# Performance work log

Hardware: AMD Instinct MI355X
Metric: run time of the kernel (lower is better)

The kernel has to match this reference:

```python
import jax, jax.numpy as jnp
import numpy as np

EPS = 1e-5


def _selective_scan(u, delta, A, Bm, Cm, D, delta_bias):
    # u, delta: (B, KD, L); A: (KD, N); Bm, Cm: (B, K, N, L); D, delta_bias: (KD,)
    Bb, KD, L = u.shape
    K = Bm.shape[1]
    Din = KD // K
    N = A.shape[1]
    delta = jax.nn.softplus(delta + delta_bias[None, :, None])            # (B,KD,L)
    dA = jnp.exp(delta[..., None] * A[None, :, None, :])                  # (B,KD,L,N)
    Bl = jnp.broadcast_to(Bm[:, :, None], (Bb, K, Din, N, L)).reshape(Bb, KD, N, L)
    Bl = jnp.moveaxis(Bl, -1, 2)                                          # (B,KD,L,N)
    dBu = (delta * u)[..., None] * Bl                                     # (B,KD,L,N)

    def comb(c1, c2):
        a1, b1 = c1
        a2, b2 = c2
        return a2 * a1, a2 * b1 + b2

    _, h = jax.lax.associative_scan(comb, (dA, dBu), axis=2)              # h: (B,KD,L,N)
    Cl = jnp.broadcast_to(Cm[:, :, None], (Bb, K, Din, N, L)).reshape(Bb, KD, N, L)
    Cl = jnp.moveaxis(Cl, -1, 2)
    y = jnp.sum(h * Cl, axis=-1) + D[None, :, None] * u                   # (B,KD,L)
    return y


def setup_inputs() -> dict:
    key = jax.random.key(0)
    ks = jax.random.split(key, 12)
    B, H, W, Dd = 1, 16, 16, 16
    C = 48            # d_model
    Din = 48          # d_inner (expand=1)
    N = 16            # d_state
    R = 3             # dt_rank = ceil(48/16)
    K = 8             # scan directions
    x = jax.random.normal(ks[0], (B, H, W, Dd, C), jnp.float32)
    in_proj_w = jax.random.normal(ks[1], (2 * Din, C), jnp.float32) * (C ** -0.5)
    conv_w = jax.random.normal(ks[2], (Din, 1, 3, 3, 3), jnp.float32) * 0.1
    conv_b = jax.random.normal(ks[3], (Din,), jnp.float32) * 0.01
    x_proj_weight = jax.random.normal(ks[4], (K, R + 2 * N, Din), jnp.float32) * (Din ** -0.5)
    dt_projs_weight = jax.random.uniform(ks[5], (K, Din, R), jnp.float32, -(R ** -0.5), R ** -0.5)
    # faithful dt bias init: inverse softplus of dt ~ logU(1e-3, 1e-1)
    u = jax.random.uniform(ks[6], (K, Din), jnp.float32)
    dt = jnp.exp(u * (np.log(0.1) - np.log(0.001)) + np.log(0.001))
    dt = jnp.clip(dt, 1e-4, None)
    dt_projs_bias = dt + jnp.log(-jnp.expm1(-dt))
    A_logs = jnp.log(jnp.broadcast_to(jnp.arange(1, N + 1, dtype=jnp.float32), (K * Din, N))).copy()
    Ds = jnp.ones((K * Din,), jnp.float32)
    norm_w = jnp.ones((Din,), jnp.float32)
    norm_b = jnp.zeros((Din,), jnp.float32)
    out_proj_w = jax.random.normal(ks[7], (C, Din), jnp.float32) * (Din ** -0.5)
    return {"x": x, "in_proj_w": in_proj_w, "conv_w": conv_w, "conv_b": conv_b,
            "x_proj_weight": x_proj_weight, "dt_projs_weight": dt_projs_weight,
            "dt_projs_bias": dt_projs_bias, "A_logs": A_logs, "Ds": Ds,
            "norm_w": norm_w, "norm_b": norm_b, "out_proj_w": out_proj_w}


def reference(x, in_proj_w, conv_w, conv_b, x_proj_weight, dt_projs_weight,
              dt_projs_bias, A_logs, Ds, norm_w, norm_b, out_proj_w):
    Bb, H, W, Dd, C = x.shape
    Din = in_proj_w.shape[0] // 2
    K = x_proj_weight.shape[0]
    R = dt_projs_weight.shape[2]
    N = A_logs.shape[1]
    L = H * W * Dd
    # in_proj and gate split
    xz = jnp.einsum('bhwdc,ec->bhwde', x, in_proj_w)
    xm, z = jnp.split(xz, 2, axis=-1)
    # depthwise 3D conv + SiLU (channels-first)
    xc = jnp.transpose(xm, (0, 4, 1, 2, 3))                               # (B,Din,H,W,D)
    xc = jax.lax.conv_general_dilated(xc, conv_w, (1, 1, 1), 'SAME',
                                      dimension_numbers=('NCDHW', 'OIDHW', 'NCDHW'),
                                      feature_group_count=Din)
    xc = jax.nn.silu(xc + conv_b[None, :, None, None, None])
    # 8 scan orderings: 4 axis permutations + their reversals
    x0 = xc.reshape(Bb, Din, L)
    x1 = jnp.transpose(xc, (0, 1, 3, 2, 4)).reshape(Bb, Din, L)
    x2 = jnp.transpose(xc, (0, 1, 4, 3, 2)).reshape(Bb, Din, L)
    x3 = jnp.transpose(xc, (0, 1, 2, 4, 3)).reshape(Bb, Din, L)
    x4s = jnp.stack([x0, x1, x2, x3], axis=1)                             # (B,4,Din,L)
    xs = jnp.concatenate([x4s, jnp.flip(x4s, axis=-1)], axis=1)           # (B,8,Din,L)
    # per-direction projections
    x_dbl = jnp.einsum('bkdl,kcd->bkcl', xs, x_proj_weight)
    dts, Bs, Cs = jnp.split(x_dbl, [R, R + N], axis=2)                    # (B,K,R,L),(B,K,N,L),(B,K,N,L)
    dts = jnp.einsum('bkrl,kdr->bkdl', dts, dt_projs_weight)              # (B,K,Din,L)
    u = xs.reshape(Bb, K * Din, L)
    delta = dts.reshape(Bb, K * Din, L)
    A = -jnp.exp(A_logs)                                                  # (K*Din, N)
    y = _selective_scan(u, delta, A, Bs, Cs, Ds, dt_projs_bias.reshape(-1))
    y = y.reshape(Bb, K, Din, L)
    # undo reversals and permutations, sum all directions
    yk = y[:, :4] + jnp.flip(y[:, 4:], axis=-1)                           # (B,4,Din,L)
    y0 = yk[:, 0].reshape(Bb, Din, H, W, Dd)
    y1 = jnp.transpose(yk[:, 1].reshape(Bb, Din, W, H, Dd), (0, 1, 3, 2, 4))
    y2 = jnp.transpose(yk[:, 2].reshape(Bb, Din, Dd, W, H), (0, 1, 4, 3, 2))
    y3 = jnp.transpose(yk[:, 3].reshape(Bb, Din, H, Dd, W), (0, 1, 2, 4, 3))
    ysum = y0 + y1 + y2 + y3                                              # (B,Din,H,W,D)
    # LayerNorm over channels, gate, out_proj
    yl = jnp.transpose(ysum, (0, 2, 3, 4, 1))                             # (B,H,W,D,Din)
    mu = jnp.mean(yl, axis=-1, keepdims=True)
    var = jnp.mean((yl - mu) ** 2, axis=-1, keepdims=True)
    yn = (yl - mu) * jax.lax.rsqrt(var + EPS) * norm_w + norm_b
    out = yn * jax.nn.silu(z)
    return jnp.einsum('bhwde,ce->bhwdc', out, out_proj_w)
```

## Files before the change

### kernel.cpp

```cpp
#include <hip/hip_runtime.h>
#include <hip/hip_bf16.h>
#include <math.h>

#define HH 16
#define WW 16
#define DD 16
#define LL 4096
#define CC 48
#define DIN 48
#define NN 16
#define RR 3
#define KK 8
#define KD 384
#define NCH 64
#define CHL 64

__device__ __forceinline__ float dpp_add(float x, const int ctrl_tag) {
    int xi = __float_as_int(x);
    int yi;
    switch (ctrl_tag) {
        case 0: yi = __builtin_amdgcn_update_dpp(0, xi, 0xB1, 0xF, 0xF, true); break;
        case 1: yi = __builtin_amdgcn_update_dpp(0, xi, 0x4E, 0xF, 0xF, true); break;
        case 2: yi = __builtin_amdgcn_update_dpp(0, xi, 0x124, 0xF, 0xF, true); break;
        default: yi = __builtin_amdgcn_update_dpp(0, xi, 0x128, 0xF, 0xF, true); break;
    }
    return x + __int_as_float(yi);
}
__device__ __forceinline__ float row16_sum(float p) {
    p = dpp_add(p, 0);
    p = dpp_add(p, 1);
    p = dpp_add(p, 2);
    p = dpp_add(p, 3);
    return p;
}

__global__ __launch_bounds__(256) void k_inproj(const float* __restrict__ x,
                                                const float* __restrict__ W,
                                                float* __restrict__ xm,
                                                float* __restrict__ z) {
    int tid = blockIdx.x * 256 + threadIdx.x;
    if (tid >= LL * 96) return;
    int e = tid % 96, l = tid / 96;
    const float4* xr = (const float4*)(x + l * CC);
    const float4* wr = (const float4*)(W + e * CC);
    float acc = 0.f;
#pragma unroll
    for (int c4 = 0; c4 < CC / 4; ++c4) {
        float4 a = xr[c4], b = wr[c4];
        acc += a.x * b.x + a.y * b.y + a.z * b.z + a.w * b.w;
    }
    if (e < DIN) xm[e * LL + l] = acc;
    else         z[l * DIN + (e - DIN)] = acc;
}

__global__ __launch_bounds__(256) void k_conv(const float* __restrict__ xm,
                                              const float* __restrict__ cw,
                                              const float* __restrict__ cb,
                                              float* __restrict__ xc) {
    int tid = blockIdx.x * 256 + threadIdx.x;
    if (tid >= DIN * LL) return;
    int s = tid & (LL - 1), d = tid >> 12;
    int dd = s & 15, w = (s >> 4) & 15, h = s >> 8;
    const float* wp = cw + d * 27;
    const float* xp = xm + d * LL;
    float acc = 0.f;
#pragma unroll
    for (int i = -1; i <= 1; ++i) {
        int hh = h + i; if (hh < 0 || hh > 15) continue;
#pragma unroll
        for (int j = -1; j <= 1; ++j) {
            int ww2 = w + j; if (ww2 < 0 || ww2 > 15) continue;
#pragma unroll
            for (int q = -1; q <= 1; ++q) {
                int dd2 = dd + q; if (dd2 < 0 || dd2 > 15) continue;
                acc += wp[(i + 1) * 9 + (j + 1) * 3 + (q + 1)]
                     * xp[hh * 256 + ww2 * 16 + dd2];
            }
        }
    }
    acc += cb[d];
    xc[tid] = acc / (1.f + __expf(-acc));
}

__global__ __launch_bounds__(768) void k_xscan1(const float* __restrict__ xc,
                                                const float* __restrict__ xpw,
                                                const float* __restrict__ dtw,
                                                const float* __restrict__ dtb,
                                                const float* __restrict__ A_logs,
                                                float* __restrict__ BC,
                                                float* __restrict__ ud_g,
                                                float* __restrict__ phf_g) {
    int k = blockIdx.x >> 6;
    int c = blockIdx.x & (NCH - 1);
    int l0 = c * CHL;
    int tid = threadIdx.x;
    __shared__ float xt[48 * 68];
    __shared__ float xd[35 * 65];
    __shared__ float2 ud[48 * 68];
    int kperm = k & 3, krev = k & 4;
#pragma unroll
    for (int r = 0; r < 4; ++r) {
        int item = r * 768 + tid;
        int d = item >> 6, i = item & 63;
        int lg = l0 + i;
        int ll = krev ? (LL - 1 - lg) : lg;
        int a = ll >> 8, b2 = (ll >> 4) & 15, c2 = ll & 15;
        int src;
        switch (kperm) {
            case 0: src = ll;                       break;
            case 1: src = b2 * 256 + a * 16 + c2;   break;
            case 2: src = c2 * 256 + b2 * 16 + a;   break;
            default: src = a * 256 + c2 * 16 + b2;  break;
        }
        xt[d * 68 + i] = xc[d * LL + src];
    }
    __syncthreads();
    if (tid < 560) {
        int cc = tid % 35, l4 = tid / 35;
        const float* wr = xpw + (k * 35 + cc) * DIN;
        float4 acc = {0.f, 0.f, 0.f, 0.f};
#pragma unroll
        for (int d2 = 0; d2 < 48; ++d2) {
            float4 v = ((const float4*)(xt + d2 * 68))[l4];
            float w = wr[d2];
            acc.x += v.x * w; acc.y += v.y * w; acc.z += v.z * w; acc.w += v.w * w;
        }
        float* o = xd + cc * 65 + l4 * 4;
        o[0] = acc.x; o[1] = acc.y; o[2] = acc.z; o[3] = acc.w;
    }
    __syncthreads();
    if (tid < 512) {
        int l = tid >> 3, q = tid & 7;
        float4 v;
#pragma unroll
        for (int j = 0; j < 4; ++j) (&v.x)[j] = xd[(3 + q * 4 + j) * 65 + l];
        ((float4*)(BC + ((size_t)(k * LL + l0 + l)) * 32))[q] = v;
    }
#pragma unroll
    for (int r = 0; r < 4; ++r) {
        int item = r * 768 + tid;
        int d2 = item >> 6, l = item & 63;
        int gd = k * DIN + d2;
        float v = xd[l] * dtw[gd * 3] + xd[65 + l] * dtw[gd * 3 + 1]
                + xd[130 + l] * dtw[gd * 3 + 2] + dtb[gd];
        float sp = (v > 20.f) ? v : log1pf(__expf(v));
        float u = xt[d2 * 68 + l];
        float2 p = make_float2(u, sp);
        ud[d2 * 68 + l] = p;
        ((float2*)ud_g)[(size_t)gd * LL + l0 + l] = p;
    }
    __syncthreads();
    int d = tid >> 4, n = tid & 15;
    int gid = k * DIN + d;
    float A = -__expf(A_logs[gid * NN + n]);
    float h = 0.f, pa = 1.f;
#pragma unroll 8
    for (int i = 0; i < CHL; ++i) {
        float2 uv = ud[d * 68 + i];
        float Bv = xd[(3 + n) * 65 + i];
        float dA = __expf(uv.y * A);
        h = h * dA + uv.y * uv.x * Bv;
        pa *= dA;
    }
    size_t si = (size_t)gid * (NCH * 16) + c * 16 + n;
    ((float2*)phf_g)[si] = make_float2(pa, h);
}

__global__ __launch_bounds__(768, 6) void k_scan3(const float* __restrict__ ud_g,
                                                  const float* __restrict__ BC,
                                                  const float* __restrict__ A_logs,
                                                  const float* __restrict__ Ds,
                                                  const float* __restrict__ phf_g,
                                                  float* __restrict__ y2) {
    int k = blockIdx.x >> 6;
    int c = blockIdx.x & (NCH - 1);
    int l0 = c * CHL;
    int tid = threadIdx.x;
    int d = tid >> 4, n = tid & 15;
    int gid = k * DIN + d;
    __shared__ float2 s_ud[48 * 64];
    __shared__ float  s_bc[64 * 32];
    __shared__ float  y_t[48 * 68];

    const float4* ud4 = (const float4*)ud_g;
    const float4* bc4 = (const float4*)BC;
    int r0 = tid >> 5, q0 = tid & 31;
    float4 ua = ud4[(size_t)(k * DIN + r0)      * (LL / 2) + (l0 / 2) + q0];
    float4 ub = ud4[(size_t)(k * DIN + 24 + r0) * (LL / 2) + (l0 / 2) + q0];
    float4 bv;
    if (tid < 512) bv = bc4[((size_t)(k * LL + l0 + (tid >> 3))) * 8 + (tid & 7)];
    ((float4*)s_ud)[tid] = ua;
    ((float4*)s_ud)[768 + tid] = ub;
    if (tid < 512) ((float4*)s_bc)[tid] = bv;

    float A = -__expf(A_logs[gid * NN + n]);
    float Dv = Ds[gid];

    float h = 0.f;
    {
        const float2* pp = ((const float2*)phf_g) + (size_t)gid * (NCH * 16) + n;
        int cc = 0;
        for (; cc + 8 <= c; cc += 8) {
            float2 v0 = pp[(cc + 0) * 16]; float2 v1 = pp[(cc + 1) * 16];
            float2 v2 = pp[(cc + 2) * 16]; float2 v3 = pp[(cc + 3) * 16];
            float2 v4 = pp[(cc + 4) * 16]; float2 v5 = pp[(cc + 5) * 16];
            float2 v6 = pp[(cc + 6) * 16]; float2 v7 = pp[(cc + 7) * 16];
            h = h * v0.x + v0.y; h = h * v1.x + v1.y;
            h = h * v2.x + v2.y; h = h * v3.x + v3.y;
            h = h * v4.x + v4.y; h = h * v5.x + v5.y;
            h = h * v6.x + v6.y; h = h * v7.x + v7.y;
        }
        for (; cc < c; ++cc) { float2 v = pp[cc * 16]; h = h * v.x + v.y; }
    }
    __syncthreads();

    const float2* ur = s_ud + d * 64;
#pragma unroll 8
    for (int i = 0; i < CHL; ++i) {
        float2 uv = ur[i];
        float Bv = s_bc[i * 32 + n];
        float Cv = s_bc[i * 32 + 16 + n];
        float dA = __expf(uv.y * A);
        h = h * dA + uv.y * uv.x * Bv;
        float p = row16_sum(h * Cv);
        if (n == 0) y_t[d * 68 + i] = p + Dv * uv.x;
    }
    __syncthreads();
    {
        int g = tid >> 6, l = tid & 63;
        int lg = l0 + l;
        int ll = (k & 4) ? (LL - 1 - lg) : lg;
        int a = ll >> 8, b2 = (ll >> 4) & 15, c2 = ll & 15;
        int s;
        switch (k & 3) {
            case 0: s = ll;                        break;
            case 1: s = b2 * 256 + a * 16 + c2;    break;
            case 2: s = c2 * 256 + b2 * 16 + a;    break;
            default: s = a * 256 + c2 * 16 + b2;   break;
        }
        float4 v;
#pragma unroll
        for (int j = 0; j < 4; ++j) (&v.x)[j] = y_t[(g * 4 + j) * 68 + l];
        ((float4*)(y2 + (size_t)s * KD + k * DIN))[g] = v;
    }
}

__global__ __launch_bounds__(256) void k_final2(const float* __restrict__ y2,
                                                const float* __restrict__ z,
                                                const float* __restrict__ nw,
                                                const float* __restrict__ nb,
                                                const float* __restrict__ opw,
                                                float* __restrict__ out) {
    int wv = threadIdx.x >> 6, lane = threadIdx.x & 63;
    int s = blockIdx.x * 4 + wv;
    __shared__ float g[4][DIN];
    float val = 0.f;
    if (lane < DIN) {
        const float* yp = y2 + (size_t)s * KD + lane;
#pragma unroll
        for (int k = 0; k < KK; ++k) val += yp[k * DIN];
    }
    float m = val;
#pragma unroll
    for (int o = 32; o >= 1; o >>= 1) m += __shfl_xor(m, o, 64);
    m *= (1.f / 48.f);
    float dv = (lane < DIN) ? (val - m) : 0.f;
    float v2 = dv * dv;
#pragma unroll
    for (int o = 32; o >= 1; o >>= 1) v2 += __shfl_xor(v2, o, 64);
    v2 *= (1.f / 48.f);
    float inv = rsqrtf(v2 + 1e-5f);
    if (lane < DIN) {
        float yn = dv * inv * nw[lane] + nb[lane];
        float zz = z[s * DIN + lane];
        g[wv][lane] = yn * (zz / (1.f + __expf(-zz)));
    }
    __syncthreads();
    if (lane < DIN) {
        const float* wr = opw + lane * DIN;
        float acc = 0.f;
#pragma unroll
        for (int e = 0; e < DIN; ++e) acc += g[wv][e] * wr[e];
        out[s * CC + lane] = acc;
    }
}

extern "C" void kernel_launch(void* const* d_in, const int* in_sizes, int n_in,
                              void* d_out, int out_size, void* d_ws, size_t ws_size,
                              hipStream_t stream) {
    const float* x      = (const float*)d_in[0];
    const float* ipw    = (const float*)d_in[1];
    const float* cw     = (const float*)d_in[2];
    const float* cb     = (const float*)d_in[3];
    const float* xpw    = (const float*)d_in[4];
    const float* dtw    = (const float*)d_in[5];
    const float* dtb    = (const float*)d_in[6];
    const float* A_logs = (const float*)d_in[7];
    const float* Ds     = (const float*)d_in[8];
    const float* nw     = (const float*)d_in[9];
    const float* nb     = (const float*)d_in[10];
    const float* opw    = (const float*)d_in[11];
    float* out = (float*)d_out;

    float* ws    = (float*)d_ws;
    float* xm    = ws;
    float* z     = xm + DIN * LL;
    float* xc    = z + LL * DIN;
    float* ud_g  = xc + DIN * LL;
    float* BC    = ud_g + (size_t)2 * KD * LL;
    float* y2    = BC + (size_t)KK * LL * 32;
    float* phf_g = y2 + (size_t)LL * KD;

    k_inproj<<<(LL * 96 + 255) / 256, 256, 0, stream>>>(x, ipw, xm, z);
    k_conv<<<(DIN * LL + 255) / 256, 256, 0, stream>>>(xm, cw, cb, xc);
    k_xscan1<<<KK * NCH, 768, 0, stream>>>(xc, xpw, dtw, dtb, A_logs,
                                           BC, ud_g, phf_g);
    k_scan3<<<KK * NCH, 768, 0, stream>>>(ud_g, BC, A_logs, Ds, phf_g, y2);
    k_final2<<<LL / 4, 256, 0, stream>>>(y2, z, nw, nb, opw, out);
}
```

Before: 143.5 us.

## Fuse scan stages and final norm into one cooperative kernel with grid syncs

Merges the chunk scan pass, the carry-propagation pass and the LayerNorm/gate/out_proj epilogue into a single cooperative kernel that uses grid.sync between phases. Shared-memory u/delta/B/C stay resident across phases, so the ud_g and BC global round trips and two launches go away. The conv kernel now tiles each channel in LDS with a padded layout and writes four pre-permuted copies of its output, so the scan reads contiguous rows instead of gathering. In exchange it relies on cooperative launch residency (512 blocks of 768 threads) and two grid barriers, with the old kernels kept as a fallback if the launch fails.

```diff
diff --git a/kernel.cpp b/kernel.cpp
--- a/kernel.cpp
+++ b/kernel.cpp
@@ -1,6 +1,8 @@
 #include <hip/hip_runtime.h>
-#include <hip/hip_bf16.h>
+#include <hip/hip_cooperative_groups.h>
 #include <math.h>
+
+namespace cg = cooperative_groups;
 
 #define HH 16
 #define WW 16
@@ -15,6 +17,8 @@
 #define NCH 64
 #define CHL 64
 
+#define OL(s) ((s) + ((s) >> 4) + ((s) >> 8))
+
 __device__ __forceinline__ float dpp_add(float x, const int ctrl_tag) {
     int xi = __float_as_int(x);
     int yi;
@@ -32,6 +36,16 @@
     p = dpp_add(p, 2);
     p = dpp_add(p, 3);
     return p;
+}
+
+__device__ __forceinline__ int perm_src(int ll, int kperm) {
+    int a = ll >> 8, b2 = (ll >> 4) & 15, c2 = ll & 15;
+    switch (kperm) {
+        case 0:  return ll;
+        case 1:  return b2 * 256 + a * 16 + c2;
+        case 2:  return c2 * 256 + b2 * 16 + a;
+        default: return a * 256 + c2 * 16 + b2;
+    }
 }
 
 __global__ __launch_bounds__(256) void k_inproj(const float* __restrict__ x,
@@ -53,33 +67,209 @@
     else         z[l * DIN + (e - DIN)] = acc;
 }
 
-__global__ __launch_bounds__(256) void k_conv(const float* __restrict__ xm,
-                                              const float* __restrict__ cw,
-                                              const float* __restrict__ cb,
-                                              float* __restrict__ xc) {
-    int tid = blockIdx.x * 256 + threadIdx.x;
-    if (tid >= DIN * LL) return;
-    int s = tid & (LL - 1), d = tid >> 12;
-    int dd = s & 15, w = (s >> 4) & 15, h = s >> 8;
+__global__ __launch_bounds__(1024) void k_conv(const float* __restrict__ xm,
+                                               const float* __restrict__ cw,
+                                               const float* __restrict__ cb,
+                                               float* __restrict__ xcp) {
+    int d = blockIdx.x;
+    int tid = threadIdx.x;
+    __shared__ float xin[4366];
+    __shared__ float xout[4366];
+    {
+        float4 v = ((const float4*)(xm + (size_t)d * LL))[tid];
+        int o = OL(tid * 4);
+        xin[o] = v.x; xin[o + 1] = v.y; xin[o + 2] = v.z; xin[o + 3] = v.w;
+    }
+    __syncthreads();
     const float* wp = cw + d * 27;
-    const float* xp = xm + d * LL;
-    float acc = 0.f;
-#pragma unroll
-    for (int i = -1; i <= 1; ++i) {
-        int hh = h + i; if (hh < 0 || hh > 15) continue;
-#pragma unroll
-        for (int j = -1; j <= 1; ++j) {
-            int ww2 = w + j; if (ww2 < 0 || ww2 > 15) continue;
-#pragma unroll
-            for (int q = -1; q <= 1; ++q) {
-                int dd2 = dd + q; if (dd2 < 0 || dd2 > 15) continue;
-                acc += wp[(i + 1) * 9 + (j + 1) * 3 + (q + 1)]
-                     * xp[hh * 256 + ww2 * 16 + dd2];
+    float bias = cb[d];
+#pragma unroll
+    for (int j = 0; j < 4; ++j) {
+        int s = tid * 4 + j;
+        int dd = s & 15, w = (s >> 4) & 15, h = s >> 8;
+        float acc = 0.f;
+#pragma unroll
+        for (int i = -1; i <= 1; ++i) {
+            int hh = h + i; if (hh < 0 || hh > 15) continue;
+#pragma unroll
+            for (int jj = -1; jj <= 1; ++jj) {
+                int ww2 = w + jj; if (ww2 < 0 || ww2 > 15) continue;
+#pragma unroll
+                for (int q = -1; q <= 1; ++q) {
+                    int dd2 = dd + q; if (dd2 < 0 || dd2 > 15) continue;
+                    acc += wp[(i + 1) * 9 + (jj + 1) * 3 + (q + 1)]
+                         * xin[OL(hh * 256 + ww2 * 16 + dd2)];
+                }
             }
         }
-    }
-    acc += cb[d];
-    xc[tid] = acc / (1.f + __expf(-acc));
+        acc += bias;
+        xout[OL(s)] = acc / (1.f + __expf(-acc));
+    }
+    __syncthreads();
+#pragma unroll
+    for (int p = 0; p < 4; ++p) {
+        float4 v;
+#pragma unroll
+        for (int j = 0; j < 4; ++j) {
+            int lp = tid * 4 + j;
+            (&v.x)[j] = xout[OL(perm_src(lp, p))];
+        }
+        ((float4*)(xcp + ((size_t)p * DIN + d) * LL))[tid] = v;
+    }
+}
+
+__global__ __launch_bounds__(768, 6) void k_mega(
+        const float* __restrict__ xcp, const float* __restrict__ xpw,
+        const float* __restrict__ dtw, const float* __restrict__ dtb,
+        const float* __restrict__ A_logs, const float* __restrict__ Ds,
+        const float* __restrict__ z,   const float* __restrict__ nw,
+        const float* __restrict__ nb,  const float* __restrict__ opw,
+        float* __restrict__ phf_g, float* __restrict__ y2,
+        float* __restrict__ out) {
+    cg::grid_group grid = cg::this_grid();
+    int k = blockIdx.x >> 6;
+    int c = blockIdx.x & (NCH - 1);
+    int l0 = c * CHL;
+    int tid = threadIdx.x;
+    int kperm = k & 3, krev = k & 4;
+    __shared__ float  xt[48 * 68];
+    __shared__ float  xd[35 * 65];
+    __shared__ float2 ud[48 * 68];
+
+    {
+        int d = tid >> 4, q = tid & 15;
+        const float* row = xcp + ((size_t)kperm * DIN + d) * LL;
+        if (!krev) {
+            float4 v = ((const float4*)(row + l0))[q];
+            xt[d * 68 + q * 4 + 0] = v.x; xt[d * 68 + q * 4 + 1] = v.y;
+            xt[d * 68 + q * 4 + 2] = v.z; xt[d * 68 + q * 4 + 3] = v.w;
+        } else {
+            float4 v = ((const float4*)(row + (LL - CHL - l0)))[15 - q];
+            xt[d * 68 + q * 4 + 3] = v.x; xt[d * 68 + q * 4 + 2] = v.y;
+            xt[d * 68 + q * 4 + 1] = v.z; xt[d * 68 + q * 4 + 0] = v.w;
+        }
+    }
+    __syncthreads();
+    if (tid < 560) {
+        int cc = tid % 35, l4 = tid / 35;
+        const float* wr = xpw + (k * 35 + cc) * DIN;
+        float4 acc = {0.f, 0.f, 0.f, 0.f};
+#pragma unroll
+        for (int d2 = 0; d2 < 48; ++d2) {
+            float4 v = ((const float4*)(xt + d2 * 68))[l4];
+            float w = wr[d2];
+            acc.x += v.x * w; acc.y += v.y * w; acc.z += v.z * w; acc.w += v.w * w;
+        }
+        float* o = xd + cc * 65 + l4 * 4;
+        o[0] = acc.x; o[1] = acc.y; o[2] = acc.z; o[3] = acc.w;
+    }
+    __syncthreads();
+#pragma unroll
+    for (int r = 0; r < 4; ++r) {
+        int item = r * 768 + tid;
+        int d2 = item >> 6, l = item & 63;
+        int gd = k * DIN + d2;
+        float v = xd[l] * dtw[gd * 3] + xd[65 + l] * dtw[gd * 3 + 1]
+                + xd[130 + l] * dtw[gd * 3 + 2] + dtb[gd];
+        float sp = (v > 20.f) ? v : log1pf(__expf(v));
+        ud[d2 * 68 + l] = make_float2(xt[d2 * 68 + l], sp);
+    }
+    __syncthreads();
+    int d = tid >> 4, n = tid & 15;
+    int gid = k * DIN + d;
+    float A = -__expf(A_logs[gid * NN + n]);
+    {
+        float h = 0.f, pa = 1.f;
+#pragma unroll 8
+        for (int i = 0; i < CHL; ++i) {
+            float2 uv = ud[d * 68 + i];
+            float Bv = xd[(3 + n) * 65 + i];
+            float dA = __expf(uv.y * A);
+            h = h * dA + uv.y * uv.x * Bv;
+            pa *= dA;
+        }
+        ((float2*)phf_g)[(size_t)gid * (NCH * 16) + c * 16 + n] =
+            make_float2(pa, h);
+    }
+
+    grid.sync();
+
+    float h = 0.f;
+    {
+        const float2* pp = ((const float2*)phf_g) + (size_t)gid * (NCH * 16) + n;
+        int cc = 0;
+        for (; cc + 8 <= c; cc += 8) {
+            float2 v0 = pp[(cc + 0) * 16]; float2 v1 = pp[(cc + 1) * 16];
+            float2 v2 = pp[(cc + 2) * 16]; float2 v3 = pp[(cc + 3) * 16];
+            float2 v4 = pp[(cc + 4) * 16]; float2 v5 = pp[(cc + 5) * 16];
+            float2 v6 = pp[(cc + 6) * 16]; float2 v7 = pp[(cc + 7) * 16];
+            h = h * v0.x + v0.y; h = h * v1.x + v1.y;
+            h = h * v2.x + v2.y; h = h * v3.x + v3.y;
+            h = h * v4.x + v4.y; h = h * v5.x + v5.y;
+            h = h * v6.x + v6.y; h = h * v7.x + v7.y;
+        }
+        for (; cc < c; ++cc) { float2 v = pp[cc * 16]; h = h * v.x + v.y; }
+    }
+    {
+        float Dv = Ds[gid];
+#pragma unroll 8
+        for (int i = 0; i < CHL; ++i) {
+            float2 uv = ud[d * 68 + i];
+            float Bv = xd[(3 + n) * 65 + i];
+            float Cv = xd[(19 + n) * 65 + i];
+            float dA = __expf(uv.y * A);
+            h = h * dA + uv.y * uv.x * Bv;
+            float p = row16_sum(h * Cv);
+            if (n == 0) xt[d * 68 + i] = p + Dv * uv.x;
+        }
+    }
+    __syncthreads();
+    {
+        int g = tid >> 6, l = tid & 63;
+        int lg = l0 + l;
+        int ll = krev ? (LL - 1 - lg) : lg;
+        int sp = perm_src(ll, kperm);
+        float4 v;
+#pragma unroll
+        for (int j = 0; j < 4; ++j) (&v.x)[j] = xt[(g * 4 + j) * 68 + l];
+        ((float4*)(y2 + (size_t)sp * KD + k * DIN))[g] = v;
+    }
+
+    grid.sync();
+
+    int wv = tid >> 6, lane = tid & 63;
+    int s = blockIdx.x * 8 + wv;
+    bool act = (wv < 8);
+    float val = 0.f;
+    if (act && lane < DIN) {
+        const float* yp = y2 + (size_t)s * KD + lane;
+#pragma unroll
+        for (int kk = 0; kk < KK; ++kk) val += yp[kk * DIN];
+    }
+    float m = val;
+#pragma unroll
+    for (int o = 32; o >= 1; o >>= 1) m += __shfl_xor(m, o, 64);
+    m *= (1.f / 48.f);
+    float dvv = (act && lane < DIN) ? (val - m) : 0.f;
+    float v2 = dvv * dvv;
+#pragma unroll
+    for (int o = 32; o >= 1; o >>= 1) v2 += __shfl_xor(v2, o, 64);
+    v2 *= (1.f / 48.f);
+    float inv = rsqrtf(v2 + 1e-5f);
+    float* gbuf = xd;
+    if (act && lane < DIN) {
+        float yn = dvv * inv * nw[lane] + nb[lane];
+        float zz = z[(size_t)s * DIN + lane];
+        gbuf[wv * DIN + lane] = yn * (zz / (1.f + __expf(-zz)));
+    }
+    __syncthreads();
+    if (act && lane < DIN) {
+        const float* wr = opw + lane * DIN;
+        float acc = 0.f;
+#pragma unroll
+        for (int e = 0; e < DIN; ++e) acc += gbuf[wv * DIN + e] * wr[e];
+        out[(size_t)s * CC + lane] = acc;
+    }
 }
 
 __global__ __launch_bounds__(768) void k_xscan1(const float* __restrict__ xc,
@@ -104,15 +294,7 @@
         int d = item >> 6, i = item & 63;
         int lg = l0 + i;
         int ll = krev ? (LL - 1 - lg) : lg;
-        int a = ll >> 8, b2 = (ll >> 4) & 15, c2 = ll & 15;
-        int src;
-        switch (kperm) {
-            case 0: src = ll;                       break;
-            case 1: src = b2 * 256 + a * 16 + c2;   break;
-            case 2: src = c2 * 256 + b2 * 16 + a;   break;
-            default: src = a * 256 + c2 * 16 + b2;  break;
-        }
-        xt[d * 68 + i] = xc[d * LL + src];
+        xt[d * 68 + i] = xc[d * LL + perm_src(ll, kperm)];
     }
     __syncthreads();
     if (tid < 560) {
@@ -162,8 +344,7 @@
         h = h * dA + uv.y * uv.x * Bv;
         pa *= dA;
     }
-    size_t si = (size_t)gid * (NCH * 16) + c * 16 + n;
-    ((float2*)phf_g)[si] = make_float2(pa, h);
+    ((float2*)phf_g)[(size_t)gid * (NCH * 16) + c * 16 + n] = make_float2(pa, h);
 }
 
 __global__ __launch_bounds__(768, 6) void k_scan3(const float* __restrict__ ud_g,
@@ -181,7 +362,6 @@
     __shared__ float2 s_ud[48 * 64];
     __shared__ float  s_bc[64 * 32];
     __shared__ float  y_t[48 * 68];
-
     const float4* ud4 = (const float4*)ud_g;
     const float4* bc4 = (const float4*)BC;
     int r0 = tid >> 5, q0 = tid & 31;
@@ -192,10 +372,8 @@
     ((float4*)s_ud)[tid] = ua;
     ((float4*)s_ud)[768 + tid] = ub;
     if (tid < 512) ((float4*)s_bc)[tid] = bv;
-
     float A = -__expf(A_logs[gid * NN + n]);
     float Dv = Ds[gid];
-
     float h = 0.f;
     {
         const float2* pp = ((const float2*)phf_g) + (size_t)gid * (NCH * 16) + n;
@@ -213,7 +391,6 @@
         for (; cc < c; ++cc) { float2 v = pp[cc * 16]; h = h * v.x + v.y; }
     }
     __syncthreads();
-
     const float2* ur = s_ud + d * 64;
 #pragma unroll 8
     for (int i = 0; i < CHL; ++i) {
@@ -230,18 +407,11 @@
         int g = tid >> 6, l = tid & 63;
         int lg = l0 + l;
         int ll = (k & 4) ? (LL - 1 - lg) : lg;
-        int a = ll >> 8, b2 = (ll >> 4) & 15, c2 = ll & 15;
-        int s;
-        switch (k & 3) {
-            case 0: s = ll;                        break;
-            case 1: s = b2 * 256 + a * 16 + c2;    break;
-            case 2: s = c2 * 256 + b2 * 16 + a;    break;
-            default: s = a * 256 + c2 * 16 + b2;   break;
-        }
+        int sp = perm_src(ll, k & 3);
         float4 v;
 #pragma unroll
         for (int j = 0; j < 4; ++j) (&v.x)[j] = y_t[(g * 4 + j) * 68 + l];
-        ((float4*)(y2 + (size_t)s * KD + k * DIN))[g] = v;
+        ((float4*)(y2 + (size_t)sp * KD + k * DIN))[g] = v;
     }
 }
 
@@ -305,16 +475,26 @@
     float* ws    = (float*)d_ws;
     float* xm    = ws;
     float* z     = xm + DIN * LL;
-    float* xc    = z + LL * DIN;
-    float* ud_g  = xc + DIN * LL;
+    float* xcp   = z + LL * DIN;
+    float* y2    = xcp + (size_t)4 * DIN * LL;
+    float* phf_g = y2 + (size_t)LL * KD;
+    float* ud_g  = phf_g + (size_t)2 * KD * NCH * 16;
     float* BC    = ud_g + (size_t)2 * KD * LL;
-    float* y2    = BC + (size_t)KK * LL * 32;
-    float* phf_g = y2 + (size_t)LL * KD;
 
     k_inproj<<<(LL * 96 + 255) / 256, 256, 0, stream>>>(x, ipw, xm, z);
-    k_conv<<<(DIN * LL + 255) / 256, 256, 0, stream>>>(xm, cw, cb, xc);
-    k_xscan1<<<KK * NCH, 768, 0, stream>>>(xc, xpw, dtw, dtb, A_logs,
-                                           BC, ud_g, phf_g);
-    k_scan3<<<KK * NCH, 768, 0, stream>>>(ud_g, BC, A_logs, Ds, phf_g, y2);
-    k_final2<<<LL / 4, 256, 0, stream>>>(y2, z, nw, nb, opw, out);
-}
+    k_conv<<<DIN, 1024, 0, stream>>>(xm, cw, cb, xcp);
+
+    void* args[] = {(void*)&xcp, (void*)&xpw, (void*)&dtw, (void*)&dtb,
+                    (void*)&A_logs, (void*)&Ds, (void*)&z, (void*)&nw,
+                    (void*)&nb, (void*)&opw, (void*)&phf_g, (void*)&y2,
+                    (void*)&out};
+    hipError_t ce = hipLaunchCooperativeKernel((void*)k_mega,
+                                               dim3(KK * NCH), dim3(768),
+                                               args, 0, stream);
+    if (ce != hipSuccess) {
+        k_xscan1<<<KK * NCH, 768, 0, stream>>>(xcp, xpw, dtw, dtb, A_logs,
+                                               BC, ud_g, phf_g);
+        k_scan3<<<KK * NCH, 768, 0, stream>>>(ud_g, BC, A_logs, Ds, phf_g, y2);
+        k_final2<<<LL / 4, 256, 0, stream>>>(y2, z, nw, nb, opw, out);
+    }
+}
```

Result: slower. 257.5 us (+79.5%).

## Recompute scan front-end in both passes and pre-permute conv output per direction

Applied to the files above, without the earlier changes.

The conv kernel now runs one block per channel, stages the volume in padded shared memory, and writes four pre-permuted copies of its output, one per scan ordering. The scan kernels can then read their inputs with contiguous float4 loads instead of gathering. The second scan kernel no longer loads stored u/delta and B/C buffers from global memory. It recomputes the x-projection, dt projection and softplus itself, which removes large intermediate writes and reads at the cost of duplicated compute. The conv launch drops to only 48 blocks, which may underuse the GPU.

```diff
diff --git a/kernel.cpp b/kernel.cpp
--- a/kernel.cpp
+++ b/kernel.cpp
@@ -1,5 +1,4 @@
 #include <hip/hip_runtime.h>
-#include <hip/hip_bf16.h>
 #include <math.h>
 
 #define HH 16
@@ -15,6 +14,8 @@
 #define NCH 64
 #define CHL 64
 
+#define OL(s) ((s) + ((s) >> 4) + ((s) >> 8))
+
 __device__ __forceinline__ float dpp_add(float x, const int ctrl_tag) {
     int xi = __float_as_int(x);
     int yi;
@@ -32,6 +33,16 @@
     p = dpp_add(p, 2);
     p = dpp_add(p, 3);
     return p;
+}
+
+__device__ __forceinline__ int perm_src(int ll, int kperm) {
+    int a = ll >> 8, b2 = (ll >> 4) & 15, c2 = ll & 15;
+    switch (kperm) {
+        case 0:  return ll;
+        case 1:  return b2 * 256 + a * 16 + c2;
+        case 2:  return c2 * 256 + b2 * 16 + a;
+        default: return a * 256 + c2 * 16 + b2;
+    }
 }
 
 __global__ __launch_bounds__(256) void k_inproj(const float* __restrict__ x,
@@ -53,66 +64,76 @@
     else         z[l * DIN + (e - DIN)] = acc;
 }
 
-__global__ __launch_bounds__(256) void k_conv(const float* __restrict__ xm,
-                                              const float* __restrict__ cw,
-                                              const float* __restrict__ cb,
-                                              float* __restrict__ xc) {
-    int tid = blockIdx.x * 256 + threadIdx.x;
-    if (tid >= DIN * LL) return;
-    int s = tid & (LL - 1), d = tid >> 12;
-    int dd = s & 15, w = (s >> 4) & 15, h = s >> 8;
+__global__ __launch_bounds__(1024) void k_conv(const float* __restrict__ xm,
+                                               const float* __restrict__ cw,
+                                               const float* __restrict__ cb,
+                                               float* __restrict__ xcp) {
+    int d = blockIdx.x;
+    int tid = threadIdx.x;
+    __shared__ float xin[4366];
+    __shared__ float xout[4366];
+    {
+        float4 v = ((const float4*)(xm + (size_t)d * LL))[tid];
+        int o = OL(tid * 4);
+        xin[o] = v.x; xin[o + 1] = v.y; xin[o + 2] = v.z; xin[o + 3] = v.w;
+    }
+    __syncthreads();
     const float* wp = cw + d * 27;
-    const float* xp = xm + d * LL;
-    float acc = 0.f;
-#pragma unroll
-    for (int i = -1; i <= 1; ++i) {
-        int hh = h + i; if (hh < 0 || hh > 15) continue;
-#pragma unroll
-        for (int j = -1; j <= 1; ++j) {
-            int ww2 = w + j; if (ww2 < 0 || ww2 > 15) continue;
-#pragma unroll
-            for (int q = -1; q <= 1; ++q) {
-                int dd2 = dd + q; if (dd2 < 0 || dd2 > 15) continue;
-                acc += wp[(i + 1) * 9 + (j + 1) * 3 + (q + 1)]
-                     * xp[hh * 256 + ww2 * 16 + dd2];
+    float bias = cb[d];
+#pragma unroll
+    for (int j = 0; j < 4; ++j) {
+        int s = tid * 4 + j;
+        int dd = s & 15, w = (s >> 4) & 15, h = s >> 8;
+        float acc = 0.f;
+#pragma unroll
+        for (int i = -1; i <= 1; ++i) {
+            int hh = h + i; if (hh < 0 || hh > 15) continue;
+#pragma unroll
+            for (int jj = -1; jj <= 1; ++jj) {
+                int ww2 = w + jj; if (ww2 < 0 || ww2 > 15) continue;
+#pragma unroll
+                for (int q = -1; q <= 1; ++q) {
+                    int dd2 = dd + q; if (dd2 < 0 || dd2 > 15) continue;
+                    acc += wp[(i + 1) * 9 + (jj + 1) * 3 + (q + 1)]
+                         * xin[OL(hh * 256 + ww2 * 16 + dd2)];
+                }
             }
         }
-    }
-    acc += cb[d];
-    xc[tid] = acc / (1.f + __expf(-acc));
-}
-
-__global__ __launch_bounds__(768) void k_xscan1(const float* __restrict__ xc,
-                                                const float* __restrict__ xpw,
-                                                const float* __restrict__ dtw,
-                                                const float* __restrict__ dtb,
-                                                const float* __restrict__ A_logs,
-                                                float* __restrict__ BC,
-                                                float* __restrict__ ud_g,
-                                                float* __restrict__ phf_g) {
-    int k = blockIdx.x >> 6;
-    int c = blockIdx.x & (NCH - 1);
-    int l0 = c * CHL;
-    int tid = threadIdx.x;
-    __shared__ float xt[48 * 68];
-    __shared__ float xd[35 * 65];
-    __shared__ float2 ud[48 * 68];
+        acc += bias;
+        xout[OL(s)] = acc / (1.f + __expf(-acc));
+    }
+    __syncthreads();
+#pragma unroll
+    for (int p = 0; p < 4; ++p) {
+        float4 v;
+#pragma unroll
+        for (int j = 0; j < 4; ++j) {
+            int lp = tid * 4 + j;
+            (&v.x)[j] = xout[OL(perm_src(lp, p))];
+        }
+        ((float4*)(xcp + ((size_t)p * DIN + d) * LL))[tid] = v;
+    }
+}
+
+__device__ __forceinline__ void frontend(const float* __restrict__ xcp,
+                                         const float* __restrict__ xpw,
+                                         const float* __restrict__ dtw,
+                                         const float* __restrict__ dtb,
+                                         int k, int l0, int tid,
+                                         float* xt, float* xd, float2* ud) {
     int kperm = k & 3, krev = k & 4;
-#pragma unroll
-    for (int r = 0; r < 4; ++r) {
-        int item = r * 768 + tid;
-        int d = item >> 6, i = item & 63;
-        int lg = l0 + i;
-        int ll = krev ? (LL - 1 - lg) : lg;
-        int a = ll >> 8, b2 = (ll >> 4) & 15, c2 = ll & 15;
-        int src;
-        switch (kperm) {
-            case 0: src = ll;                       break;
-            case 1: src = b2 * 256 + a * 16 + c2;   break;
-            case 2: src = c2 * 256 + b2 * 16 + a;   break;
-            default: src = a * 256 + c2 * 16 + b2;  break;
-        }
-        xt[d * 68 + i] = xc[d * LL + src];
+    {
+        int d = tid >> 4, q = tid & 15;
+        const float* row = xcp + ((size_t)kperm * DIN + d) * LL;
+        if (!krev) {
+            float4 v = ((const float4*)(row + l0))[q];
+            xt[d * 68 + q * 4 + 0] = v.x; xt[d * 68 + q * 4 + 1] = v.y;
+            xt[d * 68 + q * 4 + 2] = v.z; xt[d * 68 + q * 4 + 3] = v.w;
+        } else {
+            float4 v = ((const float4*)(row + (LL - CHL - l0)))[15 - q];
+            xt[d * 68 + q * 4 + 3] = v.x; xt[d * 68 + q * 4 + 2] = v.y;
+            xt[d * 68 + q * 4 + 1] = v.z; xt[d * 68 + q * 4 + 0] = v.w;
+        }
     }
     __syncthreads();
     if (tid < 560) {
@@ -129,13 +150,6 @@
         o[0] = acc.x; o[1] = acc.y; o[2] = acc.z; o[3] = acc.w;
     }
     __syncthreads();
-    if (tid < 512) {
-        int l = tid >> 3, q = tid & 7;
-        float4 v;
-#pragma unroll
-        for (int j = 0; j < 4; ++j) (&v.x)[j] = xd[(3 + q * 4 + j) * 65 + l];
-        ((float4*)(BC + ((size_t)(k * LL + l0 + l)) * 32))[q] = v;
-    }
 #pragma unroll
     for (int r = 0; r < 4; ++r) {
         int item = r * 768 + tid;
@@ -144,12 +158,25 @@
         float v = xd[l] * dtw[gd * 3] + xd[65 + l] * dtw[gd * 3 + 1]
                 + xd[130 + l] * dtw[gd * 3 + 2] + dtb[gd];
         float sp = (v > 20.f) ? v : log1pf(__expf(v));
-        float u = xt[d2 * 68 + l];
-        float2 p = make_float2(u, sp);
-        ud[d2 * 68 + l] = p;
-        ((float2*)ud_g)[(size_t)gd * LL + l0 + l] = p;
-    }
-    __syncthreads();
+        ud[d2 * 68 + l] = make_float2(xt[d2 * 68 + l], sp);
+    }
+    __syncthreads();
+}
+
+__global__ __launch_bounds__(768) void k_scanA(const float* __restrict__ xcp,
+                                               const float* __restrict__ xpw,
+                                               const float* __restrict__ dtw,
+                                               const float* __restrict__ dtb,
+                                               const float* __restrict__ A_logs,
+                                               float* __restrict__ phf_g) {
+    int k = blockIdx.x >> 6;
+    int c = blockIdx.x & (NCH - 1);
+    int l0 = c * CHL;
+    int tid = threadIdx.x;
+    __shared__ float  xt[48 * 68];
+    __shared__ float  xd[35 * 65];
+    __shared__ float2 ud[48 * 68];
+    frontend(xcp, xpw, dtw, dtb, k, l0, tid, xt, xd, ud);
     int d = tid >> 4, n = tid & 15;
     int gid = k * DIN + d;
     float A = -__expf(A_logs[gid * NN + n]);
@@ -162,40 +189,29 @@
         h = h * dA + uv.y * uv.x * Bv;
         pa *= dA;
     }
-    size_t si = (size_t)gid * (NCH * 16) + c * 16 + n;
-    ((float2*)phf_g)[si] = make_float2(pa, h);
-}
-
-__global__ __launch_bounds__(768, 6) void k_scan3(const float* __restrict__ ud_g,
-                                                  const float* __restrict__ BC,
-                                                  const float* __restrict__ A_logs,
-                                                  const float* __restrict__ Ds,
-                                                  const float* __restrict__ phf_g,
-                                                  float* __restrict__ y2) {
+    ((float2*)phf_g)[(size_t)gid * (NCH * 16) + c * 16 + n] = make_float2(pa, h);
+}
+
+__global__ __launch_bounds__(768) void k_scanB(const float* __restrict__ xcp,
+                                               const float* __restrict__ xpw,
+                                               const float* __restrict__ dtw,
+                                               const float* __restrict__ dtb,
+                                               const float* __restrict__ A_logs,
+                                               const float* __restrict__ Ds,
+                                               const float* __restrict__ phf_g,
+                                               float* __restrict__ y2) {
     int k = blockIdx.x >> 6;
     int c = blockIdx.x & (NCH - 1);
     int l0 = c * CHL;
     int tid = threadIdx.x;
+    __shared__ float  xt[48 * 68];
+    __shared__ float  xd[35 * 65];
+    __shared__ float2 ud[48 * 68];
+    frontend(xcp, xpw, dtw, dtb, k, l0, tid, xt, xd, ud);
     int d = tid >> 4, n = tid & 15;
     int gid = k * DIN + d;
-    __shared__ float2 s_ud[48 * 64];
-    __shared__ float  s_bc[64 * 32];
-    __shared__ float  y_t[48 * 68];
-
-    const float4* ud4 = (const float4*)ud_g;
-    const float4* bc4 = (const float4*)BC;
-    int r0 = tid >> 5, q0 = tid & 31;
-    float4 ua = ud4[(size_t)(k * DIN + r0)      * (LL / 2) + (l0 / 2) + q0];
-    float4 ub = ud4[(size_t)(k * DIN + 24 + r0) * (LL / 2) + (l0 / 2) + q0];
-    float4 bv;
-    if (tid < 512) bv = bc4[((size_t)(k * LL + l0 + (tid >> 3))) * 8 + (tid & 7)];
-    ((float4*)s_ud)[tid] = ua;
-    ((float4*)s_ud)[768 + tid] = ub;
-    if (tid < 512) ((float4*)s_bc)[tid] = bv;
-
     float A = -__expf(A_logs[gid * NN + n]);
     float Dv = Ds[gid];
-
     float h = 0.f;
     {
         const float2* pp = ((const float2*)phf_g) + (size_t)gid * (NCH * 16) + n;
@@ -212,36 +228,26 @@
         }
         for (; cc < c; ++cc) { float2 v = pp[cc * 16]; h = h * v.x + v.y; }
     }
-    __syncthreads();
-
-    const float2* ur = s_ud + d * 64;
 #pragma unroll 8
     for (int i = 0; i < CHL; ++i) {
-        float2 uv = ur[i];
-        float Bv = s_bc[i * 32 + n];
-        float Cv = s_bc[i * 32 + 16 + n];
+        float2 uv = ud[d * 68 + i];
+        float Bv = xd[(3 + n) * 65 + i];
+        float Cv = xd[(19 + n) * 65 + i];
         float dA = __expf(uv.y * A);
         h = h * dA + uv.y * uv.x * Bv;
         float p = row16_sum(h * Cv);
-        if (n == 0) y_t[d * 68 + i] = p + Dv * uv.x;
+        if (n == 0) xt[d * 68 + i] = p + Dv * uv.x;
     }
     __syncthreads();
     {
         int g = tid >> 6, l = tid & 63;
         int lg = l0 + l;
         int ll = (k & 4) ? (LL - 1 - lg) : lg;
-        int a = ll >> 8, b2 = (ll >> 4) & 15, c2 = ll & 15;
-        int s;
-        switch (k & 3) {
-            case 0: s = ll;                        break;
-            case 1: s = b2 * 256 + a * 16 + c2;    break;
-            case 2: s = c2 * 256 + b2 * 16 + a;    break;
-            default: s = a * 256 + c2 * 16 + b2;   break;
-        }
+        int sp = perm_src(ll, k & 3);
         float4 v;
 #pragma unroll
-        for (int j = 0; j < 4; ++j) (&v.x)[j] = y_t[(g * 4 + j) * 68 + l];
-        ((float4*)(y2 + (size_t)s * KD + k * DIN))[g] = v;
+        for (int j = 0; j < 4; ++j) (&v.x)[j] = xt[(g * 4 + j) * 68 + l];
+        ((float4*)(y2 + (size_t)sp * KD + k * DIN))[g] = v;
     }
 }
 
@@ -305,16 +311,14 @@
     float* ws    = (float*)d_ws;
     float* xm    = ws;
     float* z     = xm + DIN * LL;
-    float* xc    = z + LL * DIN;
-    float* ud_g  = xc + DIN * LL;
-    float* BC    = ud_g + (size_t)2 * KD * LL;
-    float* y2    = BC + (size_t)KK * LL * 32;
+    float* xcp   = z + LL * DIN;
+    float* y2    = xcp + (size_t)4 * DIN * LL;
     float* phf_g = y2 + (size_t)LL * KD;
 
     k_inproj<<<(LL * 96 + 255) / 256, 256, 0, stream>>>(x, ipw, xm, z);
-    k_conv<<<(DIN * LL + 255) / 256, 256, 0, stream>>>(xm, cw, cb, xc);
-    k_xscan1<<<KK * NCH, 768, 0, stream>>>(xc, xpw, dtw, dtb, A_logs,
-                                           BC, ud_g, phf_g);
-    k_scan3<<<KK * NCH, 768, 0, stream>>>(ud_g, BC, A_logs, Ds, phf_g, y2);
+    k_conv<<<DIN, 1024, 0, stream>>>(xm, cw, cb, xcp);
+    k_scanA<<<KK * NCH, 768, 0, stream>>>(xcp, xpw, dtw, dtb, A_logs, phf_g);
+    k_scanB<<<KK * NCH, 768, 0, stream>>>(xcp, xpw, dtw, dtb, A_logs, Ds,
+                                          phf_g, y2);
     k_final2<<<LL / 4, 256, 0, stream>>>(y2, z, nw, nb, opw, out);
 }
```

Result: no change. 146.2 us (+1.9%).
